# Performance work log

Measured on AMD Instinct MI355X. Metric: run time of the kernel, lower is better.

Reference implementation:

```python
import jax, jax.numpy as jnp
import numpy as np

N, D, E, EDGE_DIM, HID4 = 8192, 128, 262144, 50, 32


def setup_inputs() -> dict:
    key = jax.random.key(0)
    k = jax.random.split(key, 8)
    return {
        "mag": jax.random.uniform(k[0], (N, D), dtype=jnp.float32),
        "phase": jax.random.normal(k[1], (N, D), dtype=jnp.float32),
        "edge_index": jax.random.randint(k[2], (2, E), 0, N, dtype=jnp.int64),
        "rbf": jax.random.uniform(k[3], (E, EDGE_DIM), dtype=jnp.float32),
        "W1": jax.random.normal(k[4], (EDGE_DIM, HID4), dtype=jnp.float32) * 0.1,
        "b1": jnp.zeros((HID4,), dtype=jnp.float32),
        "W2": jax.random.normal(k[5], (HID4, 1), dtype=jnp.float32) * 0.1,
        "b2": jnp.zeros((1,), dtype=jnp.float32),
    }


def reference(mag, phase, edge_index, rbf, W1, b1, W2, b2):
    # score_ij = sum_d |z_i||z_j| cos(theta_i - theta_j) / sqrt(D)
    # cos(a-b) identity: = (mag*cos(phase)) @ (mag*cos(phase))^T + (mag*sin)@(mag*sin)^T
    scale = jnp.sqrt(jnp.asarray(mag.shape[-1], mag.dtype))
    a = mag * jnp.cos(phase)  # [N, D]
    b = mag * jnp.sin(phase)  # [N, D]
    scores = (a @ a.T + b @ b.T) / scale  # [N, N]
    # edge bias: Linear -> SiLU -> Linear -> scalar, scattered onto (i, j)
    h = jax.nn.silu(rbf @ W1 + b1)       # [E, HID4]
    bias = (h @ W2 + b2)[:, 0]           # [E]
    scores = scores.at[edge_index[0], edge_index[1]].add(bias)
    attn = jax.nn.softmax(scores, axis=1)  # softmax over keys j
    new_mag = attn @ mag
    new_phase = attn @ phase
    return new_mag, new_phase
```

## Files before the change

kernel.cpp:

```cpp
#include <hip/hip_runtime.h>
#include <hip/hip_bf16.h>

#define NN 8192
#define DD 128
#define DQK 256
#define EE 262144
#define EDGE_DIM 50
#define HID 32
#define CAP 96
#define SCALE 0.08838834764831845f
#define SCALE_LOG2E 0.12752455522410585f

using f32x4 = __attribute__((ext_vector_type(4))) float;
using f32x2 = __attribute__((ext_vector_type(2))) float;
using bf16x8 = __attribute__((ext_vector_type(8))) short;
using s16x4 = __attribute__((ext_vector_type(4))) short;

static __device__ __forceinline__ short f2b(float f) {
  __hip_bfloat16 h = __float2bfloat16(f);
  return __builtin_bit_cast(short, h);
}
static __device__ __forceinline__ float b2f(short s) {
  unsigned u = ((unsigned)(unsigned short)s) << 16;
  return __builtin_bit_cast(float, u);
}
static __device__ __forceinline__ void gll(const short* g, short* l) {
  __builtin_amdgcn_global_load_lds(
      (const __attribute__((address_space(1))) void*)g,
      (__attribute__((address_space(3))) void*)l, 16, 0, 0);
}

__global__ __launch_bounds__(256) void k1_mega(
    const float* __restrict__ mag, const float* __restrict__ phase,
    short* __restrict__ qkb, short* __restrict__ vtb,
    const float* __restrict__ rbf, const float* __restrict__ W1,
    const float* __restrict__ b1, const float* __restrict__ W2,
    const float* __restrict__ b2, const int* __restrict__ eidx,
    float* __restrict__ bias, int* __restrict__ cnt, int* __restrict__ slot) {
  __shared__ float tile[64][65];
  __shared__ alignas(16) float w1s[EDGE_DIM * HID];
  __shared__ alignas(16) float b1s[HID];
  __shared__ alignas(16) float w2s[HID];
  __shared__ float b2s;
  int b = blockIdx.x;
  int tid = threadIdx.x;
  if (b < 4096) {
    int t = b * 256 + tid;
    int n = t >> 7, d = t & 127;
    float m = mag[t], p = phase[t];
    float sn, cs;
    __sincosf(p, &sn, &cs);
    qkb[(size_t)n * DQK + d] = f2b(m * cs);
    qkb[(size_t)n * DQK + 128 + d] = f2b(m * sn);
    return;
  }
  if (b < 4608) {
    int r = b - 4096;
    int bn = r & 127, bd = (r >> 7) & 1, sel = r >> 8;
    const float* src = sel ? phase : mag;
#pragma unroll
    for (int rep = 0; rep < 16; ++rep) {
      int idx = rep * 256 + tid;
      int rr = idx >> 6, c = idx & 63;
      tile[rr][c] = src[(size_t)(bn * 64 + rr) * DD + bd * 64 + c];
    }
    __syncthreads();
#pragma unroll
    for (int rep = 0; rep < 16; ++rep) {
      int idx = rep * 256 + tid;
      int rr = idx >> 6, c = idx & 63;
      vtb[(size_t)(sel * 128 + bd * 64 + rr) * NN + bn * 64 + c] = f2b(tile[c][rr]);
    }
    return;
  }
  for (int k = tid; k < EDGE_DIM * HID; k += 256) w1s[k] = W1[k];
  if (tid < HID) { b1s[tid] = b1[tid]; w2s[tid] = W2[tid]; }
  if (tid == 0) b2s = b2[0];
  __syncthreads();
  int e = (b - 4608) * 256 + tid;
  const float* rrow = rbf + (size_t)e * EDGE_DIM;
  f32x4 r4[12];
#pragma unroll
  for (int k = 0; k < 12; ++k) r4[k] = *reinterpret_cast<const f32x4*>(rrow + 4 * k);
  f32x2 rt2 = *reinterpret_cast<const f32x2*>(rrow + 48);
  f32x4 h[8];
#pragma unroll
  for (int jj = 0; jj < 8; ++jj) h[jj] = reinterpret_cast<const f32x4*>(b1s)[jj];
#pragma unroll
  for (int k = 0; k < 12; ++k) {
#pragma unroll
    for (int qq = 0; qq < 4; ++qq) {
      const f32x4* wrow = reinterpret_cast<const f32x4*>(w1s + (4 * k + qq) * HID);
#pragma unroll
      for (int jj = 0; jj < 8; ++jj) h[jj] += r4[k][qq] * wrow[jj];
    }
  }
  {
    const f32x4* w48 = reinterpret_cast<const f32x4*>(w1s + 48 * HID);
    const f32x4* w49 = reinterpret_cast<const f32x4*>(w1s + 49 * HID);
#pragma unroll
    for (int jj = 0; jj < 8; ++jj) h[jj] += rt2.x * w48[jj] + rt2.y * w49[jj];
  }
  float outv = b2s;
#pragma unroll
  for (int jj = 0; jj < 8; ++jj) {
    f32x4 x = h[jj];
    f32x4 sl;
#pragma unroll
    for (int q = 0; q < 4; ++q) sl[q] = x[q] / (1.0f + __expf(-x[q]));
    f32x4 pr = sl * reinterpret_cast<const f32x4*>(w2s)[jj];
    outv += pr.x + pr.y + pr.z + pr.w;
  }
  bias[e] = outv;
  int i = eidx[e];
  int p = atomicAdd(&cnt[i], 1);
  if (p < CAP) slot[i * CAP + p] = e;
}

constexpr int TBM = 128;
constexpr int TBN = 128;
constexpr int PP = 136;

template <int NSPLIT>
__global__ __launch_bounds__(512, 2) void k5_flash(
    const short* __restrict__ qk,
    const short* __restrict__ vt,
    float* __restrict__ nump,
    float* __restrict__ denp) {
  constexpr int QCOLS = NN / NSPLIT;
  constexpr int NCHUNK = QCOLS / TBN;
  constexpr int GPQ = 8 / NSPLIT;
  __shared__ short Qs[TBM * 256];
  __shared__ short KV[2 * TBN * 64];
  __shared__ short Ps[TBM * PP];
  __shared__ float dl[4][TBM];
  int b = blockIdx.x;
  int q = (b & 7) / GPQ;
  int rb = (b >> 3) * GPQ + (b & (GPQ - 1));
  int tid = threadIdx.x;
  int w = tid >> 6, lane = tid & 63;
  int wr = w >> 2, wc = w & 3;
  int l15 = lane & 15, quad = lane >> 4;
  int rsw = l15 & 7;
  int wbase = w * 64;
  int r0 = rb * TBM;
  int cbase = q * QCOLS;

#pragma unroll
  for (int p = 0; p < 8; ++p) {
    int idx = p * 512 + tid;
    int row = idx >> 5, gs = idx & 31;
    gll(qk + (size_t)(r0 + row) * DQK + ((gs ^ (row & 7)) * 8),
        &Qs[(p * 512 + wbase) * 8]);
  }

  f32x4 o[4][4] = {};
  float den[4][4] = {};
  __syncthreads();

  for (int ch = 0; ch < NCHUNK; ++ch) {
    int c0 = cbase + ch * TBN;
#pragma unroll
    for (int p = 0; p < 2; ++p) {
      int idx = p * 512 + tid;
      int col = idx >> 3, gs = idx & 7;
      gll(qk + (size_t)(c0 + col) * DQK + ((gs ^ (col & 7)) * 8),
          &KV[(p * 512 + wbase) * 8]);
    }
    __syncthreads();
    f32x4 s[4][2] = {};
#pragma unroll
    for (int bk = 0; bk < 4; ++bk) {
      int buf = bk & 1;
      if (bk < 3) {
        int nb = buf ^ 1;
#pragma unroll
        for (int p = 0; p < 2; ++p) {
          int idx = p * 512 + tid;
          int col = idx >> 3, gs = idx & 7;
          gll(qk + (size_t)(c0 + col) * DQK + (bk + 1) * 64 + ((gs ^ (col & 7)) * 8),
              &KV[nb * 8192 + (p * 512 + wbase) * 8]);
        }
      }
#pragma unroll
      for (int ks = 0; ks < 2; ++ks) {
        int g = ks * 4 + quad;
        bf16x8 a[4], bb[2];
#pragma unroll
        for (int rt = 0; rt < 4; ++rt)
          a[rt] = *(const bf16x8*)&Qs[(wr * 64 + rt * 16 + l15) * 256 +
                                      ((bk * 8 + g) ^ rsw) * 8];
#pragma unroll
        for (int ct = 0; ct < 2; ++ct)
          bb[ct] = *(const bf16x8*)&KV[buf * 8192 + (wc * 32 + ct * 16 + l15) * 64 +
                                       (g ^ rsw) * 8];
#pragma unroll
        for (int rt = 0; rt < 4; ++rt)
#pragma unroll
          for (int ct = 0; ct < 2; ++ct)
            s[rt][ct] = __builtin_amdgcn_mfma_f32_16x16x32_bf16(a[rt], bb[ct],
                                                                s[rt][ct], 0, 0, 0);
      }
      __syncthreads();
    }
#pragma unroll
    for (int rt = 0; rt < 4; ++rt)
#pragma unroll
      for (int ct = 0; ct < 2; ++ct)
#pragma unroll
        for (int r = 0; r < 4; ++r) {
          float pv = exp2f(s[rt][ct][r] * SCALE_LOG2E);
          den[rt][r] += pv;
          Ps[(wr * 64 + rt * 16 + quad * 4 + r) * PP + wc * 32 + ct * 16 + l15] = f2b(pv);
        }
    __syncthreads();
#pragma unroll
    for (int jb = 0; jb < 2; ++jb) {
#pragma unroll
      for (int p = 0; p < 4; ++p) {
        int idx = p * 512 + tid;
        int feat = idx >> 3, gs = idx & 7;
        gll(vt + (size_t)feat * NN + c0 + jb * 64 + ((gs ^ (feat & 7)) * 8),
            &KV[(p * 512 + wbase) * 8]);
      }
      __syncthreads();
#pragma unroll
      for (int ks = 0; ks < 2; ++ks) {
        int g = ks * 4 + quad;
        int ko = ks * 32 + quad * 8;
        bf16x8 pa[4], vb[4];
#pragma unroll
        for (int rt = 0; rt < 4; ++rt)
          pa[rt] = *(const bf16x8*)&Ps[(wr * 64 + rt * 16 + l15) * PP + jb * 64 + ko];
#pragma unroll
        for (int ft = 0; ft < 4; ++ft)
          vb[ft] = *(const bf16x8*)&KV[(wc * 64 + ft * 16 + l15) * 64 + (g ^ rsw) * 8];
#pragma unroll
        for (int rt = 0; rt < 4; ++rt)
#pragma unroll
          for (int ft = 0; ft < 4; ++ft)
            o[rt][ft] = __builtin_amdgcn_mfma_f32_16x16x32_bf16(pa[rt], vb[ft],
                                                                o[rt][ft], 0, 0, 0);
      }
      __syncthreads();
    }
  }
  float* npB = nump + (size_t)q * NN * DQK;
#pragma unroll
  for (int rt = 0; rt < 4; ++rt)
#pragma unroll
    for (int ft = 0; ft < 4; ++ft) {
      int row = r0 + wr * 64 + rt * 16 + quad * 4;
      int feat = wc * 64 + ft * 16 + l15;
#pragma unroll
      for (int r = 0; r < 4; ++r)
        npB[(size_t)(row + r) * DQK + feat] = o[rt][ft][r];
    }
#pragma unroll
  for (int rt = 0; rt < 4; ++rt)
#pragma unroll
    for (int r = 0; r < 4; ++r) {
      float d = den[rt][r];
      d += __shfl_xor(d, 1);
      d += __shfl_xor(d, 2);
      d += __shfl_xor(d, 4);
      d += __shfl_xor(d, 8);
      if (l15 == 0) dl[wc][wr * 64 + rt * 16 + quad * 4 + r] = d;
    }
  __syncthreads();
  if (tid < TBM) {
    float d = dl[0][tid] + dl[1][tid] + dl[2][tid] + dl[3][tid];
    denp[q * NN + r0 + tid] = d;
  }
}

__global__ __launch_bounds__(256) void k6_combine(
    const int* __restrict__ eidx, const float* __restrict__ bias,
    const int* __restrict__ cntArr, const int* __restrict__ slot,
    const short* __restrict__ qk, const float* __restrict__ mag,
    const float* __restrict__ phase, const float* __restrict__ nump,
    const float* __restrict__ denp, float* __restrict__ out, int nsplit) {
  __shared__ short qs[DQK];
  __shared__ int js[CAP];
  __shared__ float bs[CAP];
  __shared__ float ess[CAP];
  __shared__ int keepf[CAP];
  __shared__ f32x4 ncl[4][64];
  __shared__ float dcl[4];
  int i = blockIdx.x;
  int tid = threadIdx.x;
  int wave = tid >> 6;
  int lane = tid & 63;
  int cnt = cntArr[i];
  if (cnt > CAP) cnt = CAP;
  if (tid < DQK) qs[tid] = qk[(size_t)i * DQK + tid];
  for (int p = tid; p < cnt; p += 256) {
    int e = slot[i * CAP + p];
    js[p] = eidx[EE + e];
    bs[p] = bias[e];
  }
  __syncthreads();
  int sub = lane & 7;
  for (int p = wave * 8 + (lane >> 3); p < cnt; p += 32) {
    int j = js[p];
    const bf16x8* kb = reinterpret_cast<const bf16x8*>(qk + (size_t)j * DQK + sub * 32);
    const bf16x8* qa = reinterpret_cast<const bf16x8*>(qs + sub * 32);
    float sp = 0.f;
#pragma unroll
    for (int t = 0; t < 4; ++t) {
      bf16x8 qv = qa[t];
      bf16x8 kv = kb[t];
#pragma unroll
      for (int u = 0; u < 8; ++u) sp += b2f(qv[u]) * b2f(kv[u]);
    }
    sp += __shfl_xor(sp, 1);
    sp += __shfl_xor(sp, 2);
    sp += __shfl_xor(sp, 4);
    if (sub == 0) ess[p] = __expf(sp * SCALE);
  }
  __syncthreads();
  {
    float bsum = 0.f;
    int keep = 0;
    if (tid < cnt) {
      int j = js[tid];
      bsum = bs[tid];
      keep = 1;
      for (int qq = 0; qq < cnt; ++qq) {
        if (qq == tid || js[qq] != j) continue;
        if (qq < tid) { keep = 0; break; }
        bsum += bs[qq];
      }
    }
    __syncthreads();
    if (tid < cnt) { bs[tid] = bsum; keepf[tid] = keep; }
    __syncthreads();
  }
  const float* vbase = (lane < 32) ? (mag + 4 * lane) : (phase + 4 * lane - 128);
  f32x4 nc = {0.f, 0.f, 0.f, 0.f};
  float denc = 0.f;
  if (wave < nsplit) {
    nc = *reinterpret_cast<const f32x4*>(nump + ((size_t)wave * NN + i) * DQK + 4 * lane);
    if (lane == 0) denc = denp[wave * NN + i];
  }
  for (int p = wave; p < cnt; p += 4) {
    if (!keepf[p]) continue;
    float delta = ess[p] * expm1f(bs[p]);
    denc += delta;
    f32x4 v = *reinterpret_cast<const f32x4*>(vbase + (size_t)js[p] * DD);
    nc += delta * v;
  }
  ncl[wave][lane] = nc;
  if (lane == 0) dcl[wave] = denc;
  __syncthreads();
  if (wave == 0) {
    f32x4 nd = ncl[0][lane] + ncl[1][lane] + ncl[2][lane] + ncl[3][lane];
    float den = dcl[0] + dcl[1] + dcl[2] + dcl[3];
    f32x4 res = nd * (1.0f / den);
    if (lane < 32)
      *reinterpret_cast<f32x4*>(out + (size_t)i * DD + 4 * lane) = res;
    else
      *reinterpret_cast<f32x4*>(out + (size_t)NN * DD + (size_t)i * DD + 4 * lane - 128) = res;
  }
}

constexpr size_t OFF_QK = 0;
constexpr size_t OFF_VT = (size_t)NN * DQK * 2;
constexpr size_t OFF_BIAS = OFF_VT + (size_t)DQK * NN * 2;
constexpr size_t OFF_CNT = OFF_BIAS + (size_t)EE * 4;
constexpr size_t OFF_SLOT = OFF_CNT + (size_t)NN * 4;
constexpr size_t OFF_NUMP = (OFF_SLOT + (size_t)NN * CAP * 4 + 255) & ~(size_t)255;
constexpr size_t WS_NEED4 = OFF_NUMP + 4ull * NN * DQK * 4 + 4ull * NN * 4;
constexpr size_t WS_NEED2 = OFF_NUMP + 2ull * NN * DQK * 4 + 2ull * NN * 4;

extern "C" void kernel_launch(void* const* d_in, const int* in_sizes, int n_in,
                              void* d_out, int out_size, void* d_ws, size_t ws_size,
                              hipStream_t stream) {
  const float* mag = (const float*)d_in[0];
  const float* phase = (const float*)d_in[1];
  const int* eidx = (const int*)d_in[2];
  const float* rbf = (const float*)d_in[3];
  const float* W1 = (const float*)d_in[4];
  const float* b1 = (const float*)d_in[5];
  const float* W2 = (const float*)d_in[6];
  const float* b2 = (const float*)d_in[7];
  float* out = (float*)d_out;
  char* ws = (char*)d_ws;
  if (ws_size < WS_NEED2) return;
  int nsplit = (ws_size >= WS_NEED4) ? 4 : 2;

  short* qkb = (short*)(ws + OFF_QK);
  short* vtb = (short*)(ws + OFF_VT);
  float* bias = (float*)(ws + OFF_BIAS);
  int* cnt = (int*)(ws + OFF_CNT);
  int* slot = (int*)(ws + OFF_SLOT);
  float* nump = (float*)(ws + OFF_NUMP);
  float* denp = (float*)(ws + OFF_NUMP + (size_t)nsplit * NN * DQK * 4);

  hipMemsetAsync(cnt, 0, (size_t)NN * 4, stream);
  k1_mega<<<5632, 256, 0, stream>>>(mag, phase, qkb, vtb, rbf, W1, b1, W2, b2,
                                    eidx, bias, cnt, slot);
  if (nsplit == 4)
    k5_flash<4><<<(NN / TBM) * 4, 512, 0, stream>>>(qkb, vtb, nump, denp);
  else
    k5_flash<2><<<(NN / TBM) * 2, 512, 0, stream>>>(qkb, vtb, nump, denp);
  k6_combine<<<NN, 256, 0, stream>>>(eidx, bias, cnt, slot, qkb, mag, phase, nump,
                                     denp, out, nsplit);
}
```

Measured before the change: 304.8 us.

## Halve flash query tile to 64 rows and XOR-swizzle P buffer for occupancy

Shrinks the query row tile of the flash kernel from 128 to 64 rows and raises the launch-bounds occupancy hint from 2 to 4 blocks. This halves per-thread accumulators and LDS use. The P staging buffer loses its padded stride in favor of an XOR-swizzled layout, and the denominator scratch now reuses the KV buffer instead of a separate array. Together these are meant to allow more resident waves to hide latency, at the cost of reloading each K/V chunk for twice as many row blocks, which doubles K/V global and LDS traffic.

Result: faster. 292.8 us (-3.9%).

```diff
diff --git a/kernel.cpp b/kernel.cpp
--- a/kernel.cpp
+++ b/kernel.cpp
@@ -117,12 +117,11 @@
   if (p < CAP) slot[i * CAP + p] = e;
 }
 
-constexpr int TBM = 128;
+constexpr int TBM = 64;
 constexpr int TBN = 128;
-constexpr int PP = 136;
 
 template <int NSPLIT>
-__global__ __launch_bounds__(512, 2) void k5_flash(
+__global__ __launch_bounds__(512, 4) void k5_flash(
     const short* __restrict__ qk,
     const short* __restrict__ vt,
     float* __restrict__ nump,
@@ -130,10 +129,9 @@
   constexpr int QCOLS = NN / NSPLIT;
   constexpr int NCHUNK = QCOLS / TBN;
   constexpr int GPQ = 8 / NSPLIT;
-  __shared__ short Qs[TBM * 256];
-  __shared__ short KV[2 * TBN * 64];
-  __shared__ short Ps[TBM * PP];
-  __shared__ float dl[4][TBM];
+  __shared__ alignas(16) short Qs[TBM * 256];
+  __shared__ alignas(16) short KV[2 * TBN * 64];
+  __shared__ alignas(16) short Ps[TBM * 128];
   int b = blockIdx.x;
   int q = (b & 7) / GPQ;
   int rb = (b >> 3) * GPQ + (b & (GPQ - 1));
@@ -147,15 +145,15 @@
   int cbase = q * QCOLS;
 
 #pragma unroll
-  for (int p = 0; p < 8; ++p) {
+  for (int p = 0; p < 4; ++p) {
     int idx = p * 512 + tid;
     int row = idx >> 5, gs = idx & 31;
     gll(qk + (size_t)(r0 + row) * DQK + ((gs ^ (row & 7)) * 8),
         &Qs[(p * 512 + wbase) * 8]);
   }
 
-  f32x4 o[4][4] = {};
-  float den[4][4] = {};
+  f32x4 o[2][4] = {};
+  float den[2][4] = {};
   __syncthreads();
 
   for (int ch = 0; ch < NCHUNK; ++ch) {
@@ -168,7 +166,7 @@
           &KV[(p * 512 + wbase) * 8]);
     }
     __syncthreads();
-    f32x4 s[4][2] = {};
+    f32x4 s[2][2] = {};
 #pragma unroll
     for (int bk = 0; bk < 4; ++bk) {
       int buf = bk & 1;
@@ -185,17 +183,17 @@
 #pragma unroll
       for (int ks = 0; ks < 2; ++ks) {
         int g = ks * 4 + quad;
-        bf16x8 a[4], bb[2];
-#pragma unroll
-        for (int rt = 0; rt < 4; ++rt)
-          a[rt] = *(const bf16x8*)&Qs[(wr * 64 + rt * 16 + l15) * 256 +
+        bf16x8 a[2], bb[2];
+#pragma unroll
+        for (int rt = 0; rt < 2; ++rt)
+          a[rt] = *(const bf16x8*)&Qs[(wr * 32 + rt * 16 + l15) * 256 +
                                       ((bk * 8 + g) ^ rsw) * 8];
 #pragma unroll
         for (int ct = 0; ct < 2; ++ct)
           bb[ct] = *(const bf16x8*)&KV[buf * 8192 + (wc * 32 + ct * 16 + l15) * 64 +
                                        (g ^ rsw) * 8];
 #pragma unroll
-        for (int rt = 0; rt < 4; ++rt)
+        for (int rt = 0; rt < 2; ++rt)
 #pragma unroll
           for (int ct = 0; ct < 2; ++ct)
             s[rt][ct] = __builtin_amdgcn_mfma_f32_16x16x32_bf16(a[rt], bb[ct],
@@ -204,15 +202,19 @@
       __syncthreads();
     }
 #pragma unroll
-    for (int rt = 0; rt < 4; ++rt)
-#pragma unroll
-      for (int ct = 0; ct < 2; ++ct)
+    for (int rt = 0; rt < 2; ++rt)
+#pragma unroll
+      for (int ct = 0; ct < 2; ++ct) {
+        int col = wc * 32 + ct * 16 + l15;
+        int cg = col >> 3, co = col & 7;
 #pragma unroll
         for (int r = 0; r < 4; ++r) {
           float pv = exp2f(s[rt][ct][r] * SCALE_LOG2E);
           den[rt][r] += pv;
-          Ps[(wr * 64 + rt * 16 + quad * 4 + r) * PP + wc * 32 + ct * 16 + l15] = f2b(pv);
+          int row = wr * 32 + rt * 16 + quad * 4 + r;
+          Ps[row * 128 + ((cg ^ (row & 7)) * 8 + co)] = f2b(pv);
         }
+      }
     __syncthreads();
 #pragma unroll
     for (int jb = 0; jb < 2; ++jb) {
@@ -227,16 +229,18 @@
 #pragma unroll
       for (int ks = 0; ks < 2; ++ks) {
         int g = ks * 4 + quad;
-        int ko = ks * 32 + quad * 8;
-        bf16x8 pa[4], vb[4];
-#pragma unroll
-        for (int rt = 0; rt < 4; ++rt)
-          pa[rt] = *(const bf16x8*)&Ps[(wr * 64 + rt * 16 + l15) * PP + jb * 64 + ko];
+        bf16x8 pa[2], vb[4];
+#pragma unroll
+        for (int rt = 0; rt < 2; ++rt) {
+          int row = wr * 32 + rt * 16 + l15;
+          pa[rt] = *(const bf16x8*)&Ps[row * 128 +
+                                       (((jb * 8 + g) ^ (row & 7)) * 8)];
+        }
 #pragma unroll
         for (int ft = 0; ft < 4; ++ft)
           vb[ft] = *(const bf16x8*)&KV[(wc * 64 + ft * 16 + l15) * 64 + (g ^ rsw) * 8];
 #pragma unroll
-        for (int rt = 0; rt < 4; ++rt)
+        for (int rt = 0; rt < 2; ++rt)
 #pragma unroll
           for (int ft = 0; ft < 4; ++ft)
             o[rt][ft] = __builtin_amdgcn_mfma_f32_16x16x32_bf16(pa[rt], vb[ft],
@@ -247,17 +251,18 @@
   }
   float* npB = nump + (size_t)q * NN * DQK;
 #pragma unroll
-  for (int rt = 0; rt < 4; ++rt)
+  for (int rt = 0; rt < 2; ++rt)
 #pragma unroll
     for (int ft = 0; ft < 4; ++ft) {
-      int row = r0 + wr * 64 + rt * 16 + quad * 4;
+      int row = r0 + wr * 32 + rt * 16 + quad * 4;
       int feat = wc * 64 + ft * 16 + l15;
 #pragma unroll
       for (int r = 0; r < 4; ++r)
         npB[(size_t)(row + r) * DQK + feat] = o[rt][ft][r];
     }
-#pragma unroll
-  for (int rt = 0; rt < 4; ++rt)
+  float* dl = reinterpret_cast<float*>(KV);
+#pragma unroll
+  for (int rt = 0; rt < 2; ++rt)
 #pragma unroll
     for (int r = 0; r < 4; ++r) {
       float d = den[rt][r];
@@ -265,11 +270,12 @@
       d += __shfl_xor(d, 2);
       d += __shfl_xor(d, 4);
       d += __shfl_xor(d, 8);
-      if (l15 == 0) dl[wc][wr * 64 + rt * 16 + quad * 4 + r] = d;
+      if (l15 == 0) dl[wc * TBM + wr * 32 + rt * 16 + quad * 4 + r] = d;
     }
   __syncthreads();
   if (tid < TBM) {
-    float d = dl[0][tid] + dl[1][tid] + dl[2][tid] + dl[3][tid];
+    float d = dl[0 * TBM + tid] + dl[1 * TBM + tid] + dl[2 * TBM + tid] +
+              dl[3 * TBM + tid];
     denp[q * NN + r0 + tid] = d;
   }
 }
```
